# Optimization experiments

Hardware: AMD Instinct MI355X
Metric: run time of the kernel (lower is better)

Reference implementation:

```python
import jax, jax.numpy as jnp
import numpy as np

B, S, E, H, DK = 2, 1024, 1024, 128, 8  # batch, seq, embed_dim, num_heads, d_k (= n_wires)


def setup_inputs() -> dict:
    key = jax.random.key(0)
    ks = jax.random.split(key, 10)
    sc = 1.0 / np.sqrt(E)
    inp = {
        "x": jax.random.normal(ks[0], (B, S, E), dtype=jnp.float32),
        "Wq": jax.random.normal(ks[1], (E, E), dtype=jnp.float32) * sc,
        "bq": jnp.zeros((E,), jnp.float32),
        "Wk": jax.random.normal(ks[2], (E, E), dtype=jnp.float32) * sc,
        "bk": jnp.zeros((E,), jnp.float32),
        "Wv": jax.random.normal(ks[3], (E, E), dtype=jnp.float32) * sc,
        "bv": jnp.zeros((E,), jnp.float32),
        "phi": jax.random.uniform(ks[4], (H, DK), jnp.float32, -np.pi, np.pi),  # trainable RX angles per head
        "Wo": jax.random.normal(ks[5], (E, E), dtype=jnp.float32) * sc,
        "bo": jnp.zeros((E,), jnp.float32),
    }
    return inp


def reference(x, Wq, bq, Wk, bk, Wv, bv, phi, Wo, bo):
    b, s, e = x.shape
    h, dk = phi.shape
    # QKV projections (k, v are computed but unused in the original forward)
    q = (x @ Wq.T + bq).reshape(b, s, h, dk).transpose(0, 2, 1, 3)  # [B,H,S,DK]
    k = (x @ Wk.T + bk).reshape(b, s, h, dk).transpose(0, 2, 1, 3)
    v = (x @ Wv.T + bv).reshape(b, s, h, dk).transpose(0, 2, 1, 3)
    del k, v  # dead in original math
    # Quantum circuit per head: RX(q_i) then RX(phi_i) on |0>, measure PauliZ.
    # RX angles on same wire add; <Z> after RX(theta)|0> = cos(theta).
    out = jnp.cos(q + phi[None, :, None, :])  # [B,H,S,DK]
    scores = jnp.einsum("bhsd,bhtd->bhst", out, out) / np.sqrt(dk)
    attn = jax.nn.softmax(scores, axis=-1)  # dropout is identity in eval mode
    ctx = jnp.einsum("bhst,bhtd->bhsd", attn, out)
    ctx = ctx.transpose(0, 2, 1, 3).reshape(b, s, e)
    return ctx @ Wo.T + bo
```

## Files before the change

kernel.cpp:

```cpp
#include <hip/hip_runtime.h>
#include <hip/hip_bf16.h>

#define Bv  2
#define Sv  1024
#define Ev  1024
#define Hv  128
#define DKv 8
#define Mv  (Bv*Sv)

typedef __attribute__((ext_vector_type(8))) short short8;
typedef __attribute__((ext_vector_type(4))) float f32x4;

static __device__ __forceinline__ short f2b(float f) {
    __hip_bfloat16 h = __float2bfloat16(f);
    return *reinterpret_cast<short*>(&h);
}

static __device__ __forceinline__ unsigned cvtpk(float a, float b) {
    unsigned r;
    asm("v_cvt_pk_bf16_f32 %0, %1, %2" : "=v"(r) : "v"(a), "v"(b));
    return r;
}

static __device__ __forceinline__ float hexp2(float x) {
    return __builtin_amdgcn_exp2f(x);
}

static __device__ __forceinline__ void gload16(const void* g, void* l) {
    __builtin_amdgcn_global_load_lds(
        (const __attribute__((address_space(1))) unsigned int*)g,
        (__attribute__((address_space(3))) unsigned int*)l, 16, 0, 0);
}

__global__ __launch_bounds__(256)
void cvt_bf16(const float* __restrict__ in, short* __restrict__ out, int n8)
{
    const int i = blockIdx.x * 256 + threadIdx.x;
    if (i >= n8) return;
    float4 a = ((const float4*)in)[2 * i];
    float4 b = ((const float4*)in)[2 * i + 1];
    uint4 o;
    o.x = cvtpk(a.x, a.y); o.y = cvtpk(a.z, a.w);
    o.z = cvtpk(b.x, b.y); o.w = cvtpk(b.z, b.w);
    ((uint4*)out)[i] = o;
}

template<int EPI>
__global__ __launch_bounds__(256)
void gemm_bf16(const short* __restrict__ A, const short* __restrict__ W,
               const float* __restrict__ bias, const float* __restrict__ phi,
               void* __restrict__ outv)
{
    __shared__ short As[128 * 64];
    __shared__ short Bs[64 * 64];

    const int t    = threadIdx.x;
    const int w    = t >> 6, lane = t & 63;
    const int c    = lane & 15, g = lane >> 4;
    const int wr   = w >> 1,  wc = w & 1;
    const int tm   = blockIdx.y * 128, tn = blockIdx.x * 64;
    const int lr   = lane >> 3;
    const int lc   = (lane & 7) * 8;

    f32x4 acc[4][2] = {};

    for (int k0 = 0; k0 < Ev; k0 += 64) {
        #pragma unroll
        for (int j = 0; j < 4; j++) {
            const int row = w * 32 + j * 8;
            gload16(&A[(size_t)(tm + row + lr) * Ev + k0 + lc], &As[row * 64]);
        }
        #pragma unroll
        for (int j = 0; j < 2; j++) {
            const int row = w * 16 + j * 8;
            gload16(&W[(size_t)(tn + row + lr) * Ev + k0 + lc], &Bs[row * 64]);
        }
        __syncthreads();

        #pragma unroll
        for (int kk = 0; kk < 64; kk += 32) {
            short8 af[4], bf[2];
            #pragma unroll
            for (int m = 0; m < 4; m++)
                af[m] = *(const short8*)&As[(wr * 64 + m * 16 + c) * 64 + kk + 8 * g];
            #pragma unroll
            for (int n = 0; n < 2; n++)
                bf[n] = *(const short8*)&Bs[(wc * 32 + n * 16 + c) * 64 + kk + 8 * g];
            #pragma unroll
            for (int m = 0; m < 4; m++)
                #pragma unroll
                for (int n = 0; n < 2; n++)
                    acc[m][n] = __builtin_amdgcn_mfma_f32_16x16x32_bf16(af[m], bf[n], acc[m][n], 0, 0, 0);
        }
        __syncthreads();
    }

    #pragma unroll
    for (int i = 0; i < 4; i++) {
        #pragma unroll
        for (int j = 0; j < 2; j++) {
            const int n = tn + wc * 32 + j * 16 + c;
            #pragma unroll
            for (int r = 0; r < 4; r++) {
                const int m = tm + wr * 64 + i * 16 + 4 * g + r;
                const float v = acc[i][j][r];
                if (EPI == 0) {
                    float q = __cosf(v + bias[n] + phi[n]);
                    const int bb = m >> 10, ss = m & (Sv - 1);
                    const int hh = n >> 3,  dd = n & (DKv - 1);
                    ((short*)outv)[(((size_t)bb * Hv + hh) * Sv + ss) * DKv + dd] = f2b(q);
                } else {
                    ((float*)outv)[(size_t)m * Ev + n] = v + bias[n];
                }
            }
        }
    }
}

__global__ __launch_bounds__(256)
void attn_mfma(const short* __restrict__ om, short* __restrict__ ctx)
{
    __shared__ short K_lds[Sv * DKv];
    __shared__ short Vt[DKv * 1032];
    __shared__ short P_lds[4][16][40];

    const int t  = threadIdx.x;
    const int bh = blockIdx.x;
    const short* base = om + (size_t)bh * (Sv * DKv);

    #pragma unroll
    for (int r = 0; r < 4; r++) {
        const int k = r * 256 + t;
        int4 row = ((const int4*)base)[k];
        ((int4*)K_lds)[k] = row;
        union { int4 v; short s[8]; } u; u.v = row;
        #pragma unroll
        for (int d = 0; d < 8; d++) Vt[d * 1032 + k] = u.s[d];
    }
    __syncthreads();

    const int w = t >> 6, lane = t & 63;
    const int c = lane & 15, g = lane >> 4;
    const int q0 = blockIdx.y * 64 + w * 16;

    short8 qf = {};
    if (g == 0) qf = *(const short8*)&K_lds[(q0 + c) * 8];

    f32x4 ctx_acc = {0.f, 0.f, 0.f, 0.f};
    float lsum = 0.f;

    for (int kt = 0; kt < Sv; kt += 32) {
        short8 kf0 = {}, kf1 = {};
        if (g == 0) {
            kf0 = *(const short8*)&K_lds[(kt +      c) * 8];
            kf1 = *(const short8*)&K_lds[(kt + 16 + c) * 8];
        }
        const f32x4 z = {0.f, 0.f, 0.f, 0.f};
        f32x4 s0 = __builtin_amdgcn_mfma_f32_16x16x32_bf16(kf0, qf, z, 0, 0, 0);
        f32x4 s1 = __builtin_amdgcn_mfma_f32_16x16x32_bf16(kf1, qf, z, 0, 0, 0);

        float p[8];
        #pragma unroll
        for (int r = 0; r < 4; r++) {
            p[r]     = hexp2(s0[r] * 0.5100697f);
            p[4 + r] = hexp2(s1[r] * 0.5100697f);
        }
        lsum += ((p[0] + p[1]) + (p[2] + p[3])) + ((p[4] + p[5]) + (p[6] + p[7]));

        uint2 w0, w1;
        w0.x = cvtpk(p[0], p[1]); w0.y = cvtpk(p[2], p[3]);
        w1.x = cvtpk(p[4], p[5]); w1.y = cvtpk(p[6], p[7]);
        *(uint2*)&P_lds[w][c][4 * g]      = w0;
        *(uint2*)&P_lds[w][c][16 + 4 * g] = w1;

        short8 pf = *(const short8*)&P_lds[w][c][8 * g];
        short8 vf = {};
        if (c < 8) vf = *(const short8*)&Vt[c * 1032 + kt + 8 * g];
        ctx_acc = __builtin_amdgcn_mfma_f32_16x16x32_bf16(pf, vf, ctx_acc, 0, 0, 0);
    }

    lsum += __shfl_xor(lsum, 16);
    lsum += __shfl_xor(lsum, 32);
    float L[4];
    #pragma unroll
    for (int r = 0; r < 4; r++) L[r] = __shfl(lsum, 4 * g + r);

    if (c < 8) {
        const int b = bh >> 7, h = bh & (Hv - 1);
        #pragma unroll
        for (int r = 0; r < 4; r++) {
            const int q = q0 + 4 * g + r;
            ctx[((size_t)(b * Sv + q)) * Ev + h * DKv + c] = f2b(ctx_acc[r] / L[r]);
        }
    }
}

extern "C" void kernel_launch(void* const* d_in, const int* in_sizes, int n_in,
                              void* d_out, int out_size, void* d_ws, size_t ws_size,
                              hipStream_t stream)
{
    const float* x   = (const float*)d_in[0];
    const float* Wq  = (const float*)d_in[1];
    const float* bq  = (const float*)d_in[2];
    const float* phi = (const float*)d_in[7];
    const float* Wo  = (const float*)d_in[8];
    const float* bo  = (const float*)d_in[9];
    float* out = (float*)d_out;

    char* ws = (char*)d_ws;
    short* xb  = (short*)ws;
    short* ctx = xb;
    short* om  = (short*)(ws + (4 << 20));
    short* Wqb = (short*)(ws + (8 << 20));
    short* Wob = (short*)(ws + (10 << 20));

    cvt_bf16<<<dim3(Mv * Ev / 2048), 256, 0, stream>>>(x,  xb,  Mv * Ev / 8);
    cvt_bf16<<<dim3(Ev * Ev / 2048), 256, 0, stream>>>(Wq, Wqb, Ev * Ev / 8);
    cvt_bf16<<<dim3(Ev * Ev / 2048), 256, 0, stream>>>(Wo, Wob, Ev * Ev / 8);

    const dim3 gg(Ev / 64, Mv / 128);
    gemm_bf16<0><<<gg, 256, 0, stream>>>(xb, Wqb, bq, phi, (void*)om);
    attn_mfma<<<dim3(Bv * Hv, Sv / 64), 256, 0, stream>>>(om, ctx);
    gemm_bf16<1><<<gg, 256, 0, stream>>>(ctx, Wob, bo, nullptr, (void*)out);
}
```

Baseline: 184.7 us.

## Merge conversion launches, double-buffer GEMM tiles with XOR swizzle, shrink tile

The three fp32-to-bf16 conversion launches are merged into one kernel that picks its source by block index, saving two launches. The GEMM drops to a 64x64 tile, which doubles the grid from 256 to 512 blocks on the many-CU GPU. It also double-buffers the LDS stages so the next K-slice loads while the current one is computed, and XOR-swizzles the LDS column layout to avoid bank conflicts. The trade-off is less data reuse per block, and the single barrier per iteration may leave a race on the buffer being refilled.

Result: faster. 174.1 us (-5.7%).

```diff
diff --git a/kernel.cpp b/kernel.cpp
--- a/kernel.cpp
+++ b/kernel.cpp
@@ -33,16 +33,21 @@
 }
 
 __global__ __launch_bounds__(256)
-void cvt_bf16(const float* __restrict__ in, short* __restrict__ out, int n8)
-{
-    const int i = blockIdx.x * 256 + threadIdx.x;
-    if (i >= n8) return;
-    float4 a = ((const float4*)in)[2 * i];
-    float4 b = ((const float4*)in)[2 * i + 1];
+void cvt_all(const float* __restrict__ x, const float* __restrict__ wq,
+             const float* __restrict__ wo, short* __restrict__ xb,
+             short* __restrict__ wqb, short* __restrict__ wob)
+{
+    const int b = blockIdx.x;
+    const float* src; short* dst; int i;
+    if (b < 1024)      { src = x;  dst = xb;  i = b * 256 + threadIdx.x; }
+    else if (b < 1536) { src = wq; dst = wqb; i = (b - 1024) * 256 + threadIdx.x; }
+    else               { src = wo; dst = wob; i = (b - 1536) * 256 + threadIdx.x; }
+    float4 a = ((const float4*)src)[2 * i];
+    float4 c = ((const float4*)src)[2 * i + 1];
     uint4 o;
     o.x = cvtpk(a.x, a.y); o.y = cvtpk(a.z, a.w);
-    o.z = cvtpk(b.x, b.y); o.w = cvtpk(b.z, b.w);
-    ((uint4*)out)[i] = o;
+    o.z = cvtpk(c.x, c.y); o.w = cvtpk(c.z, c.w);
+    ((uint4*)dst)[i] = o;
 }
 
 template<int EPI>
@@ -51,43 +56,46 @@
                const float* __restrict__ bias, const float* __restrict__ phi,
                void* __restrict__ outv)
 {
-    __shared__ short As[128 * 64];
-    __shared__ short Bs[64 * 64];
+    __shared__ short As[2][64 * 64];
+    __shared__ short Bs[2][64 * 64];
 
     const int t    = threadIdx.x;
     const int w    = t >> 6, lane = t & 63;
     const int c    = lane & 15, g = lane >> 4;
+    const int cs   = c & 7;
     const int wr   = w >> 1,  wc = w & 1;
-    const int tm   = blockIdx.y * 128, tn = blockIdx.x * 64;
+    const int tm   = blockIdx.y * 64, tn = blockIdx.x * 64;
     const int lr   = lane >> 3;
-    const int lc   = (lane & 7) * 8;
-
-    f32x4 acc[4][2] = {};
-
-    for (int k0 = 0; k0 < Ev; k0 += 64) {
-        #pragma unroll
-        for (int j = 0; j < 4; j++) {
-            const int row = w * 32 + j * 8;
-            gload16(&A[(size_t)(tm + row + lr) * Ev + k0 + lc], &As[row * 64]);
-        }
-        #pragma unroll
-        for (int j = 0; j < 2; j++) {
-            const int row = w * 16 + j * 8;
-            gload16(&W[(size_t)(tn + row + lr) * Ev + k0 + lc], &Bs[row * 64]);
-        }
-        __syncthreads();
-
+    const int lcs  = ((lane & 7) ^ lr) * 8;
+
+    f32x4 acc[2][2] = {};
+
+    #define STAGE(s, k0)                                                        \
+        _Pragma("unroll")                                                       \
+        for (int j = 0; j < 2; j++) {                                           \
+            const int row = w * 16 + j * 8;                                     \
+            gload16(&A[(size_t)(tm + row + lr) * Ev + (k0) + lcs], &As[s][row * 64]); \
+            gload16(&W[(size_t)(tn + row + lr) * Ev + (k0) + lcs], &Bs[s][row * 64]); \
+        }
+
+    STAGE(0, 0)
+    __syncthreads();
+
+    for (int ks = 0; ks < 16; ks++) {
+        const int cur = ks & 1;
+        if (ks < 15) { STAGE(cur ^ 1, (ks + 1) * 64) }
         #pragma unroll
         for (int kk = 0; kk < 64; kk += 32) {
-            short8 af[4], bf[2];
-            #pragma unroll
-            for (int m = 0; m < 4; m++)
-                af[m] = *(const short8*)&As[(wr * 64 + m * 16 + c) * 64 + kk + 8 * g];
+            const int s0 = ((kk >> 3) + g) ^ cs;
+            short8 af[2], bf[2];
+            #pragma unroll
+            for (int m = 0; m < 2; m++)
+                af[m] = *(const short8*)&As[cur][(wr * 32 + m * 16 + c) * 64 + s0 * 8];
             #pragma unroll
             for (int n = 0; n < 2; n++)
-                bf[n] = *(const short8*)&Bs[(wc * 32 + n * 16 + c) * 64 + kk + 8 * g];
-            #pragma unroll
-            for (int m = 0; m < 4; m++)
+                bf[n] = *(const short8*)&Bs[cur][(wc * 32 + n * 16 + c) * 64 + s0 * 8];
+            #pragma unroll
+            for (int m = 0; m < 2; m++)
                 #pragma unroll
                 for (int n = 0; n < 2; n++)
                     acc[m][n] = __builtin_amdgcn_mfma_f32_16x16x32_bf16(af[m], bf[n], acc[m][n], 0, 0, 0);
@@ -96,13 +104,13 @@
     }
 
     #pragma unroll
-    for (int i = 0; i < 4; i++) {
+    for (int i = 0; i < 2; i++) {
         #pragma unroll
         for (int j = 0; j < 2; j++) {
             const int n = tn + wc * 32 + j * 16 + c;
             #pragma unroll
             for (int r = 0; r < 4; r++) {
-                const int m = tm + wr * 64 + i * 16 + 4 * g + r;
+                const int m = tm + wr * 32 + i * 16 + 4 * g + r;
                 const float v = acc[i][j][r];
                 if (EPI == 0) {
                     float q = __cosf(v + bias[n] + phi[n]);
@@ -115,6 +123,7 @@
             }
         }
     }
+    #undef STAGE
 }
 
 __global__ __launch_bounds__(256)
@@ -214,11 +223,9 @@
     short* Wqb = (short*)(ws + (8 << 20));
     short* Wob = (short*)(ws + (10 << 20));
 
-    cvt_bf16<<<dim3(Mv * Ev / 2048), 256, 0, stream>>>(x,  xb,  Mv * Ev / 8);
-    cvt_bf16<<<dim3(Ev * Ev / 2048), 256, 0, stream>>>(Wq, Wqb, Ev * Ev / 8);
-    cvt_bf16<<<dim3(Ev * Ev / 2048), 256, 0, stream>>>(Wo, Wob, Ev * Ev / 8);
-
-    const dim3 gg(Ev / 64, Mv / 128);
+    cvt_all<<<dim3(2048), 256, 0, stream>>>(x, Wq, Wo, xb, Wqb, Wob);
+
+    const dim3 gg(Ev / 64, Mv / 64);
     gemm_bf16<0><<<gg, 256, 0, stream>>>(xb, Wqb, bq, phi, (void*)om);
     attn_mfma<<<dim3(Bv * Hv, Sv / 64), 256, 0, stream>>>(om, ctx);
     gemm_bf16<1><<<gg, 256, 0, stream>>>(ctx, Wob, bo, nullptr, (void*)out);
```
